# Kernel tuning notes

Measured on AMD Instinct MI355X. Metric: run time of the kernel, lower is better.

Reference implementation:

```python
import jax, jax.numpy as jnp
import numpy as np

D_MODEL = 1024
N_HEAD = 16
B, S = 4, 1024


def setup_inputs() -> dict:
    key = jax.random.key(0)
    ks = jax.random.split(key, 10)
    f = lambda k, shp: jax.random.normal(k, shp, dtype=jnp.float32)
    return {
        "x": f(ks[0], (B, S, D_MODEL)),
        "y": f(ks[1], (B, S, D_MODEL)),
        "z": f(ks[2], (B, S, D_MODEL)),
        "mask": f(ks[3], (1, 1, S, S)) * 0.1,
        "wq_w": f(ks[4], (D_MODEL, D_MODEL)) * (D_MODEL ** -0.5),
        "wq_b": f(ks[5], (D_MODEL,)) * 0.02,
        "wk_w": f(ks[6], (D_MODEL, D_MODEL)) * (D_MODEL ** -0.5),
        "wk_b": f(ks[7], (D_MODEL,)) * 0.02,
        "wv_w": f(ks[8], (D_MODEL, D_MODEL)) * (D_MODEL ** -0.5),
        "wv_b": f(ks[9], (D_MODEL,)) * 0.02,
    }


def reference(x, y, z, mask, wq_w, wq_b, wk_w, wk_b, wv_w, wv_b):
    b, xl, d = x.shape
    hd = d // N_HEAD
    # linear projections (torch Linear: x @ W^T + b)
    q = x @ wq_w.T + wq_b
    k = y @ wk_w.T + wk_b
    v = z @ wv_w.T + wv_b
    # [B, H, L, hd]
    q = q.reshape(b, xl, N_HEAD, hd).transpose(0, 2, 1, 3)
    k = k.reshape(b, y.shape[1], N_HEAD, hd).transpose(0, 2, 1, 3)
    v = v.reshape(b, z.shape[1], N_HEAD, hd).transpose(0, 2, 1, 3)
    # NOTE: source scales by sqrt(d_model), not sqrt(head_dim)
    scale = 1.0 / jnp.sqrt(jnp.asarray(d, dtype=x.dtype))
    logits = jnp.einsum("bhqd,bhkd->bhqk", q, k) * scale
    score = jax.nn.softmax(logits, axis=-1)
    # mask added AFTER softmax (faithful to source)
    score = score + mask
    out = jnp.einsum("bhqk,bhkd->bhqd", score, v)
    return out.transpose(0, 2, 1, 3).reshape(b, xl, d)
```

## Files before the change

kernel.cpp:

```cpp
#include <hip/hip_runtime.h>
#include <hip/hip_bf16.h>
#include <cstdint>

typedef __bf16 bf16_t;
typedef __bf16 bf16x8 __attribute__((ext_vector_type(8)));
typedef __bf16 bf16x4 __attribute__((ext_vector_type(4)));
typedef float floatx4 __attribute__((ext_vector_type(4)));
typedef float floatx16 __attribute__((ext_vector_type(16)));
typedef uint32_t u32x4 __attribute__((ext_vector_type(4)));

typedef __attribute__((address_space(3))) uint32_t lds_u32_t;
typedef const __attribute__((address_space(1))) uint32_t g_u32_t;

#define MFMA_BF16(a, b, c) __builtin_amdgcn_mfma_f32_16x16x32_bf16((a), (b), (c), 0, 0, 0)
#define MFMA32_BF16(a, b, c) __builtin_amdgcn_mfma_f32_32x32x16_bf16((a), (b), (c), 0, 0, 0)

#if __has_builtin(__builtin_amdgcn_exp2f)
#define EXP2F(x) __builtin_amdgcn_exp2f(x)
#else
#define EXP2F(x) __expf((x) * 0.6931471805599453f)
#endif

static constexpr int S = 1024;
static constexpr int HD = 64;

struct ConvArgs {
  const float* src[7];
  bf16_t* dst[7];
  int n[7];
};

__global__ __launch_bounds__(256) void convert_kernel(ConvArgs a) {
  const int j = blockIdx.y;
  const float4* __restrict__ s = (const float4*)a.src[j];
  bf16x8* __restrict__ d = (bf16x8*)a.dst[j];
  const int n8 = a.n[j] >> 3;
  for (int i = blockIdx.x * blockDim.x + threadIdx.x; i < n8; i += gridDim.x * blockDim.x) {
    float4 v0 = s[2 * i];
    float4 v1 = s[2 * i + 1];
    bf16x8 o;
    o[0] = (bf16_t)v0.x; o[1] = (bf16_t)v0.y; o[2] = (bf16_t)v0.z; o[3] = (bf16_t)v0.w;
    o[4] = (bf16_t)v1.x; o[5] = (bf16_t)v1.y; o[6] = (bf16_t)v1.z; o[7] = (bf16_t)v1.w;
    d[i] = o;
  }
}

struct GemmCfg {
  const bf16_t* A;
  const bf16_t* Bm;
  void* out;
  const float* bias;
  int mode;
  float scale;
};

union GemmSmem {
  struct { bf16_t A[128 * 64]; bf16_t B[128 * 64]; } ab;
  bf16_t C[128 * 136];
};

__global__ __launch_bounds__(256, 3) void gemm_nt_kernel(GemmCfg c0, GemmCfg c1, GemmCfg c2, int K) {
  GemmCfg cfg = (blockIdx.y == 0) ? c0 : (blockIdx.y == 1 ? c1 : c2);
  __shared__ GemmSmem u;
  __shared__ float bias_s[128];
  const int tid = threadIdx.x;
  const int wave = tid >> 6;
  const int lane = tid & 63;
  const int g = lane >> 4;
  const int cl = lane & 15;
  const int mq = (wave & 1) * 64;
  const int nq = (wave >> 1) * 64;

  const int xcd = blockIdx.x & 7, idx = blockIdx.x >> 3;
  int mb, nb;
  if (cfg.mode == 0) { mb = xcd * 4 + (idx & 3); nb = idx >> 2; }
  else               { nb = xcd * 4 + (idx & 3); mb = idx >> 2; }
  const int m0 = mb * 128, n0 = nb * 128;

  if (tid < 128) bias_s[tid] = cfg.bias[(cfg.mode == 0 ? n0 : m0) + tid];

  const int srow = tid >> 3;
  const int sch = (tid & 7) ^ (srow & 7);
  const bf16_t* Ag = cfg.A + (size_t)(m0 + srow) * K + sch * 8;
  const bf16_t* Bg = cfg.Bm + (size_t)(n0 + srow) * K + sch * 8;
  const int swz = cl & 7;

  floatx4 acc[4][4];
#pragma unroll
  for (int i = 0; i < 4; ++i)
#pragma unroll
    for (int j = 0; j < 4; ++j) acc[i][j] = floatx4{0.f, 0.f, 0.f, 0.f};

  const int kiters = K >> 6;
  for (int kt = 0; kt < kiters; ++kt) {
    __syncthreads();
#pragma unroll
    for (int i = 0; i < 4; ++i) {
      __builtin_amdgcn_global_load_lds((g_u32_t*)(const void*)(Ag + (size_t)(i * 32) * K),
                                       (lds_u32_t*)(void*)&u.ab.A[(i * 256 + tid) * 8], 16, 0, 0);
      __builtin_amdgcn_global_load_lds((g_u32_t*)(const void*)(Bg + (size_t)(i * 32) * K),
                                       (lds_u32_t*)(void*)&u.ab.B[(i * 256 + tid) * 8], 16, 0, 0);
    }
    Ag += 64;
    Bg += 64;
    __syncthreads();

#pragma unroll
    for (int kc = 0; kc < 2; ++kc) {
      bf16x8 af[4], bfr[4];
#pragma unroll
      for (int i = 0; i < 4; ++i)
        af[i] = *(const bf16x8*)&u.ab.A[(mq + i * 16 + cl) * 64 + ((kc * 4 + g) ^ swz) * 8];
#pragma unroll
      for (int j = 0; j < 4; ++j)
        bfr[j] = *(const bf16x8*)&u.ab.B[(nq + j * 16 + cl) * 64 + ((kc * 4 + g) ^ swz) * 8];
#pragma unroll
      for (int i = 0; i < 4; ++i)
#pragma unroll
        for (int j = 0; j < 4; ++j) acc[i][j] = MFMA_BF16(af[i], bfr[j], acc[i][j]);
    }
  }

  __syncthreads();
#pragma unroll
  for (int i = 0; i < 4; ++i)
#pragma unroll
    for (int j = 0; j < 4; ++j)
#pragma unroll
      for (int r = 0; r < 4; ++r) {
        const int ml = mq + i * 16 + g * 4 + r;
        const int nl = nq + j * 16 + cl;
        float v = (acc[i][j][r] + bias_s[cfg.mode == 0 ? nl : ml]) * cfg.scale;
        u.C[ml * 136 + nl] = (bf16_t)v;
      }
  __syncthreads();
#pragma unroll
  for (int it = 0; it < 8; ++it) {
    const int ix = it * 256 + tid;
    const int ml = ix >> 4, nc = ix & 15;
    bf16x8 val = *(const bf16x8*)&u.C[ml * 136 + nc * 8];
    const int m = m0 + ml, n = n0 + nc * 8;
    size_t addr;
    if (cfg.mode == 0)
      addr = (size_t)((m >> 10) * 16 + (n >> 6)) * 65536 + (m & 1023) * 64 + (n & 63);
    else
      addr = (size_t)((n >> 10) * 16 + (m >> 6)) * 65536 + (m & 63) * 1024 + (n & 1023);
    *(bf16x8*)&((bf16_t*)cfg.out)[addr] = val;
  }
}

__global__ __launch_bounds__(256, 2) void attn_kernel(const bf16_t* __restrict__ Q,
                                                      const bf16_t* __restrict__ Kb,
                                                      const bf16_t* __restrict__ Vt,
                                                      const bf16_t* __restrict__ Mk,
                                                      float* __restrict__ out) {
  __shared__ bf16_t Ks[128 * 64];
  __shared__ bf16_t Vs[64 * 128];
  const int tid = threadIdx.x;
  const int wave = tid >> 6, lane = tid & 63;
  const int l31 = lane & 31, hi = lane >> 5;
  const int bh = blockIdx.x & 63, qt = blockIdx.x >> 6;
  const int q0w = qt * 128 + wave * 32;
  const bf16_t* Qp = Q + (size_t)bh * (S * HD);
  const bf16_t* Kp = Kb + (size_t)bh * (S * HD);
  const bf16_t* Vp = Vt + (size_t)bh * (S * HD);
  const bf16_t* Mp = Mk + (size_t)(q0w + l31) * S;

  const int krow = tid >> 3, kch = (tid & 7) ^ (krow & 7);
  const int vrow = tid >> 4, vch = (tid & 15) ^ (vrow & 7);
  const int swk = l31 & 7;

  bf16x8 qf[4];
#pragma unroll
  for (int kk = 0; kk < 4; ++kk)
    qf[kk] = *(const bf16x8*)&Qp[(size_t)(q0w + l31) * HD + kk * 16 + hi * 8];

  floatx16 o[2], o2[2];
#pragma unroll
  for (int nt = 0; nt < 2; ++nt) {
#pragma unroll
    for (int r = 0; r < 16; ++r) { o[nt][r] = 0.f; o2[nt][r] = 0.f; }
  }
  float dsq = 0.f;

  for (int kt = 0; kt < 8; ++kt) {
    const int k0 = kt * 128;
    __syncthreads();
#pragma unroll
    for (int i = 0; i < 4; ++i)
      __builtin_amdgcn_global_load_lds(
          (g_u32_t*)(const void*)&Kp[(size_t)(k0 + i * 32 + krow) * HD + kch * 8],
          (lds_u32_t*)(void*)&Ks[(i * 256 + tid) * 8], 16, 0, 0);
#pragma unroll
    for (int i = 0; i < 4; ++i)
      __builtin_amdgcn_global_load_lds(
          (g_u32_t*)(const void*)&Vp[(size_t)(i * 16 + vrow) * S + k0 + vch * 8],
          (lds_u32_t*)(void*)&Vs[(i * 256 + tid) * 8], 16, 0, 0);

    bf16x8 mf[8];
#pragma unroll
    for (int kc = 0; kc < 8; ++kc)
      mf[kc] = *(const bf16x8*)&Mp[k0 + kc * 16 + hi * 8];
    __syncthreads();

    floatx16 s[4];
#pragma unroll
    for (int mt = 0; mt < 4; ++mt) {
#pragma unroll
      for (int r = 0; r < 16; ++r) s[mt][r] = 0.f;
#pragma unroll
      for (int kk = 0; kk < 4; ++kk) {
        bf16x8 kf = *(const bf16x8*)&Ks[(mt * 32 + l31) * 64 + ((kk * 2 + hi) ^ swk) * 8];
        s[mt] = MFMA32_BF16(kf, qf[kk], s[mt]);
      }
    }

    bf16x8 pf[8];
#pragma unroll
    for (int mt = 0; mt < 4; ++mt) {
      float e[16];
#pragma unroll
      for (int r = 0; r < 16; ++r) {
        e[r] = EXP2F(s[mt][r]);
        dsq += e[r];
      }
      uint32_t c[8];
#pragma unroll
      for (int i = 0; i < 8; ++i) {
        bf16_t lo = (bf16_t)e[2 * i], hh = (bf16_t)e[2 * i + 1];
        c[i] = (uint32_t)__builtin_bit_cast(uint16_t, lo) |
               ((uint32_t)__builtin_bit_cast(uint16_t, hh) << 16);
      }
      asm volatile("v_permlane32_swap_b32 %0, %1" : "+v"(c[0]), "+v"(c[2]));
      asm volatile("v_permlane32_swap_b32 %0, %1" : "+v"(c[1]), "+v"(c[3]));
      asm volatile("v_permlane32_swap_b32 %0, %1" : "+v"(c[4]), "+v"(c[6]));
      asm volatile("v_permlane32_swap_b32 %0, %1" : "+v"(c[5]), "+v"(c[7]));
      u32x4 pe = {c[0], c[1], c[2], c[3]};
      u32x4 po = {c[4], c[5], c[6], c[7]};
      pf[2 * mt] = __builtin_bit_cast(bf16x8, pe);
      pf[2 * mt + 1] = __builtin_bit_cast(bf16x8, po);
    }

#pragma unroll
    for (int kc = 0; kc < 8; ++kc) {
#pragma unroll
      for (int nt = 0; nt < 2; ++nt) {
        bf16x8 vf = *(const bf16x8*)&Vs[(nt * 32 + l31) * 128 + ((kc * 2 + hi) ^ swk) * 8];
        o[nt] = MFMA32_BF16(pf[kc], vf, o[nt]);
        o2[nt] = MFMA32_BF16(mf[kc], vf, o2[nt]);
      }
    }
  }

  dsq += __shfl_xor(dsq, 32, 64);
  float dinv = 1.0f / dsq;

  const int b = bh >> 4, h = bh & 15;
#pragma unroll
  for (int r = 0; r < 16; ++r) {
    const int qr = (r & 3) + 8 * (r >> 2) + 4 * hi;
    float dv = __builtin_bit_cast(
        float, __builtin_amdgcn_ds_bpermute(qr << 2, __builtin_bit_cast(int, dinv)));
    const int srow = q0w + qr;
#pragma unroll
    for (int nt = 0; nt < 2; ++nt)
      out[((size_t)b * S + srow) * 1024 + h * HD + nt * 32 + l31] = o[nt][r] * dv + o2[nt][r];
  }
}

extern "C" void kernel_launch(void* const* d_in, const int* in_sizes, int n_in,
                              void* d_out, int out_size, void* d_ws, size_t ws_size,
                              hipStream_t stream) {
  const float* x = (const float*)d_in[0];
  const float* y = (const float*)d_in[1];
  const float* z = (const float*)d_in[2];
  const float* mask = (const float*)d_in[3];
  const float* wq_w = (const float*)d_in[4];
  const float* wq_b = (const float*)d_in[5];
  const float* wk_w = (const float*)d_in[6];
  const float* wk_b = (const float*)d_in[7];
  const float* wv_w = (const float*)d_in[8];
  const float* wv_b = (const float*)d_in[9];

  uint8_t* ws = (uint8_t*)d_ws;
  const size_t MB = 1u << 20;
  bf16_t* Xb = (bf16_t*)(ws + 0 * MB);
  bf16_t* Yb = (bf16_t*)(ws + 8 * MB);
  bf16_t* Zb = (bf16_t*)(ws + 16 * MB);
  bf16_t* Wqb = (bf16_t*)(ws + 24 * MB);
  bf16_t* Wkb = (bf16_t*)(ws + 26 * MB);
  bf16_t* Wvb = (bf16_t*)(ws + 28 * MB);
  bf16_t* Mb = (bf16_t*)(ws + 30 * MB);
  bf16_t* Qb = (bf16_t*)(ws + 32 * MB);
  bf16_t* Kb = (bf16_t*)(ws + 40 * MB);
  bf16_t* Vtb = (bf16_t*)(ws + 48 * MB);

  ConvArgs ca;
  ca.src[0] = x;    ca.dst[0] = Xb;  ca.n[0] = 4 * 1024 * 1024;
  ca.src[1] = y;    ca.dst[1] = Yb;  ca.n[1] = 4 * 1024 * 1024;
  ca.src[2] = z;    ca.dst[2] = Zb;  ca.n[2] = 4 * 1024 * 1024;
  ca.src[3] = wq_w; ca.dst[3] = Wqb; ca.n[3] = 1024 * 1024;
  ca.src[4] = wk_w; ca.dst[4] = Wkb; ca.n[4] = 1024 * 1024;
  ca.src[5] = wv_w; ca.dst[5] = Wvb; ca.n[5] = 1024 * 1024;
  ca.src[6] = mask; ca.dst[6] = Mb;  ca.n[6] = 1024 * 1024;
  convert_kernel<<<dim3(512, 7), 256, 0, stream>>>(ca);

  const float qscale = 0.0450842200277801f;
  GemmCfg cq{Xb, Wqb, (void*)Qb, wq_b, 0, qscale};
  GemmCfg ck{Yb, Wkb, (void*)Kb, wk_b, 0, 1.0f};
  GemmCfg cv{Wvb, Zb, (void*)Vtb, wv_b, 1, 1.0f};
  gemm_nt_kernel<<<dim3(256, 3), 256, 0, stream>>>(cq, ck, cv, 1024);

  attn_kernel<<<dim3(512), 256, 0, stream>>>(Qb, Kb, Vtb, Mb, (float*)d_out);
}
```

Before: 181.2 us.

## Split mask@V into separate GEMM and double-buffer K/V tiles in attention

The post-softmax mask term (mask @ V) moves out of the attention kernel into a new batched mode of the projection GEMM, which writes an fp32 intermediate that attention adds in its epilogue. Attention drops the per-tile mask loads and half of its P·V MFMAs, and it now double-buffers the K/V LDS tiles so the next tile's loads overlap the current tile's compute. The row-sum accumulation also becomes a tree reduction. In exchange there is an extra kernel launch, a 16 MB fp32 write and read round-trip through global memory, and twice the LDS per attention block.

```diff
diff --git a/kernel.cpp b/kernel.cpp
--- a/kernel.cpp
+++ b/kernel.cpp
@@ -72,17 +72,19 @@
   const int nq = (wave >> 1) * 64;
 
   const int xcd = blockIdx.x & 7, idx = blockIdx.x >> 3;
-  int mb, nb;
-  if (cfg.mode == 0) { mb = xcd * 4 + (idx & 3); nb = idx >> 2; }
-  else               { nb = xcd * 4 + (idx & 3); mb = idx >> 2; }
+  int mb, nb, batch = 0;
+  if (cfg.mode == 0)      { mb = xcd * 4 + (idx & 3); nb = idx >> 2; }
+  else if (cfg.mode == 1) { nb = xcd * 4 + (idx & 3); mb = idx >> 2; }
+  else                    { nb = xcd; mb = idx & 7; batch = idx >> 3; }
   const int m0 = mb * 128, n0 = nb * 128;
 
-  if (tid < 128) bias_s[tid] = cfg.bias[(cfg.mode == 0 ? n0 : m0) + tid];
+  const bf16_t* Bbase = cfg.Bm + (size_t)batch * (1u << 20);
+  if (cfg.mode != 2 && tid < 128) bias_s[tid] = cfg.bias[(cfg.mode == 0 ? n0 : m0) + tid];
 
   const int srow = tid >> 3;
   const int sch = (tid & 7) ^ (srow & 7);
   const bf16_t* Ag = cfg.A + (size_t)(m0 + srow) * K + sch * 8;
-  const bf16_t* Bg = cfg.Bm + (size_t)(n0 + srow) * K + sch * 8;
+  const bf16_t* Bg = Bbase + (size_t)(n0 + srow) * K + sch * 8;
   const int swz = cl & 7;
 
   floatx4 acc[4][4];
@@ -119,6 +121,21 @@
 #pragma unroll
         for (int j = 0; j < 4; ++j) acc[i][j] = MFMA_BF16(af[i], bfr[j], acc[i][j]);
     }
+  }
+
+  if (cfg.mode == 2) {
+    float* O = (float*)cfg.out + (size_t)batch * (1u << 20);
+#pragma unroll
+    for (int i = 0; i < 4; ++i)
+#pragma unroll
+      for (int j = 0; j < 4; ++j)
+#pragma unroll
+        for (int r = 0; r < 4; ++r) {
+          const int ml = m0 + mq + i * 16 + g * 4 + r;
+          const int nl = n0 + nq + j * 16 + cl;
+          O[(size_t)ml * 1024 + nl] = acc[i][j][r];
+        }
+    return;
   }
 
   __syncthreads();
@@ -152,10 +169,10 @@
 __global__ __launch_bounds__(256, 2) void attn_kernel(const bf16_t* __restrict__ Q,
                                                       const bf16_t* __restrict__ Kb,
                                                       const bf16_t* __restrict__ Vt,
-                                                      const bf16_t* __restrict__ Mk,
+                                                      const float* __restrict__ O2,
                                                       float* __restrict__ out) {
-  __shared__ bf16_t Ks[128 * 64];
-  __shared__ bf16_t Vs[64 * 128];
+  __shared__ bf16_t Ks[2][128 * 64];
+  __shared__ bf16_t Vs[2][64 * 128];
   const int tid = threadIdx.x;
   const int wave = tid >> 6, lane = tid & 63;
   const int l31 = lane & 31, hi = lane >> 5;
@@ -164,44 +181,45 @@
   const bf16_t* Qp = Q + (size_t)bh * (S * HD);
   const bf16_t* Kp = Kb + (size_t)bh * (S * HD);
   const bf16_t* Vp = Vt + (size_t)bh * (S * HD);
-  const bf16_t* Mp = Mk + (size_t)(q0w + l31) * S;
 
   const int krow = tid >> 3, kch = (tid & 7) ^ (krow & 7);
   const int vrow = tid >> 4, vch = (tid & 15) ^ (vrow & 7);
   const int swk = l31 & 7;
 
+#define STAGE(BUF, KT)                                                                      \
+  do {                                                                                      \
+    const int k0s = (KT) * 128;                                                             \
+    _Pragma("unroll") for (int i = 0; i < 4; ++i)                                           \
+        __builtin_amdgcn_global_load_lds(                                                   \
+            (g_u32_t*)(const void*)&Kp[(size_t)(k0s + i * 32 + krow) * HD + kch * 8],       \
+            (lds_u32_t*)(void*)&Ks[BUF][(i * 256 + tid) * 8], 16, 0, 0);                    \
+    _Pragma("unroll") for (int i = 0; i < 4; ++i)                                           \
+        __builtin_amdgcn_global_load_lds(                                                   \
+            (g_u32_t*)(const void*)&Vp[(size_t)(i * 16 + vrow) * S + k0s + vch * 8],        \
+            (lds_u32_t*)(void*)&Vs[BUF][(i * 256 + tid) * 8], 16, 0, 0);                    \
+  } while (0)
+
   bf16x8 qf[4];
 #pragma unroll
   for (int kk = 0; kk < 4; ++kk)
     qf[kk] = *(const bf16x8*)&Qp[(size_t)(q0w + l31) * HD + kk * 16 + hi * 8];
 
-  floatx16 o[2], o2[2];
-#pragma unroll
-  for (int nt = 0; nt < 2; ++nt) {
-#pragma unroll
-    for (int r = 0; r < 16; ++r) { o[nt][r] = 0.f; o2[nt][r] = 0.f; }
-  }
+  floatx16 o[2];
+#pragma unroll
+  for (int nt = 0; nt < 2; ++nt)
+#pragma unroll
+    for (int r = 0; r < 16; ++r) o[nt][r] = 0.f;
   float dsq = 0.f;
 
+  STAGE(0, 0);
+  __syncthreads();
+
+  int cur = 0;
   for (int kt = 0; kt < 8; ++kt) {
-    const int k0 = kt * 128;
-    __syncthreads();
-#pragma unroll
-    for (int i = 0; i < 4; ++i)
-      __builtin_amdgcn_global_load_lds(
-          (g_u32_t*)(const void*)&Kp[(size_t)(k0 + i * 32 + krow) * HD + kch * 8],
-          (lds_u32_t*)(void*)&Ks[(i * 256 + tid) * 8], 16, 0, 0);
-#pragma unroll
-    for (int i = 0; i < 4; ++i)
-      __builtin_amdgcn_global_load_lds(
-          (g_u32_t*)(const void*)&Vp[(size_t)(i * 16 + vrow) * S + k0 + vch * 8],
-          (lds_u32_t*)(void*)&Vs[(i * 256 + tid) * 8], 16, 0, 0);
-
-    bf16x8 mf[8];
-#pragma unroll
-    for (int kc = 0; kc < 8; ++kc)
-      mf[kc] = *(const bf16x8*)&Mp[k0 + kc * 16 + hi * 8];
-    __syncthreads();
+    if (kt < 7) STAGE(cur ^ 1, kt + 1);
+
+    const bf16_t* Kc = &Ks[cur][0];
+    const bf16_t* Vc = &Vs[cur][0];
 
     floatx16 s[4];
 #pragma unroll
@@ -210,7 +228,7 @@
       for (int r = 0; r < 16; ++r) s[mt][r] = 0.f;
 #pragma unroll
       for (int kk = 0; kk < 4; ++kk) {
-        bf16x8 kf = *(const bf16x8*)&Ks[(mt * 32 + l31) * 64 + ((kk * 2 + hi) ^ swk) * 8];
+        bf16x8 kf = *(const bf16x8*)&Kc[(mt * 32 + l31) * 64 + ((kk * 2 + hi) ^ swk) * 8];
         s[mt] = MFMA32_BF16(kf, qf[kk], s[mt]);
       }
     }
@@ -220,10 +238,12 @@
     for (int mt = 0; mt < 4; ++mt) {
       float e[16];
 #pragma unroll
-      for (int r = 0; r < 16; ++r) {
-        e[r] = EXP2F(s[mt][r]);
-        dsq += e[r];
-      }
+      for (int r = 0; r < 16; ++r) e[r] = EXP2F(s[mt][r]);
+      float t0 = (e[0] + e[1]) + (e[2] + e[3]);
+      float t1 = (e[4] + e[5]) + (e[6] + e[7]);
+      float t2 = (e[8] + e[9]) + (e[10] + e[11]);
+      float t3 = (e[12] + e[13]) + (e[14] + e[15]);
+      dsq += (t0 + t1) + (t2 + t3);
       uint32_t c[8];
 #pragma unroll
       for (int i = 0; i < 8; ++i) {
@@ -245,17 +265,21 @@
     for (int kc = 0; kc < 8; ++kc) {
 #pragma unroll
       for (int nt = 0; nt < 2; ++nt) {
-        bf16x8 vf = *(const bf16x8*)&Vs[(nt * 32 + l31) * 128 + ((kc * 2 + hi) ^ swk) * 8];
+        bf16x8 vf = *(const bf16x8*)&Vc[(nt * 32 + l31) * 128 + ((kc * 2 + hi) ^ swk) * 8];
         o[nt] = MFMA32_BF16(pf[kc], vf, o[nt]);
-        o2[nt] = MFMA32_BF16(mf[kc], vf, o2[nt]);
       }
     }
-  }
+
+    __syncthreads();
+    cur ^= 1;
+  }
+#undef STAGE
 
   dsq += __shfl_xor(dsq, 32, 64);
   float dinv = 1.0f / dsq;
 
   const int b = bh >> 4, h = bh & 15;
+  const float* O2p = O2 + ((size_t)b * S) * 1024 + h * HD;
 #pragma unroll
   for (int r = 0; r < 16; ++r) {
     const int qr = (r & 3) + 8 * (r >> 2) + 4 * hi;
@@ -263,8 +287,11 @@
         float, __builtin_amdgcn_ds_bpermute(qr << 2, __builtin_bit_cast(int, dinv)));
     const int srow = q0w + qr;
 #pragma unroll
-    for (int nt = 0; nt < 2; ++nt)
-      out[((size_t)b * S + srow) * 1024 + h * HD + nt * 32 + l31] = o[nt][r] * dv + o2[nt][r];
+    for (int nt = 0; nt < 2; ++nt) {
+      const int col = nt * 32 + l31;
+      out[((size_t)b * S + srow) * 1024 + h * HD + col] =
+          o[nt][r] * dv + O2p[(size_t)srow * 1024 + col];
+    }
   }
 }
 
@@ -294,6 +321,7 @@
   bf16_t* Qb = (bf16_t*)(ws + 32 * MB);
   bf16_t* Kb = (bf16_t*)(ws + 40 * MB);
   bf16_t* Vtb = (bf16_t*)(ws + 48 * MB);
+  float* O2f = (float*)(ws + 56 * MB);
 
   ConvArgs ca;
   ca.src[0] = x;    ca.dst[0] = Xb;  ca.n[0] = 4 * 1024 * 1024;
@@ -311,5 +339,8 @@
   GemmCfg cv{Wvb, Zb, (void*)Vtb, wv_b, 1, 1.0f};
   gemm_nt_kernel<<<dim3(256, 3), 256, 0, stream>>>(cq, ck, cv, 1024);
 
-  attn_kernel<<<dim3(512), 256, 0, stream>>>(Qb, Kb, Vtb, Mb, (float*)d_out);
+  GemmCfg cm{Mb, Vtb, (void*)O2f, wq_b, 2, 1.0f};
+  gemm_nt_kernel<<<dim3(256, 1), 256, 0, stream>>>(cm, cm, cm, 1024);
+
+  attn_kernel<<<dim3(512), 256, 0, stream>>>(Qb, Kb, Vtb, O2f, (float*)d_out);
 }
```

Result: slower. 191.4 us (+5.7%).
